# Kernel tuning notes

Hardware: AMD Instinct MI355X
Metric: run time of the kernel (lower is better)

The kernel has to match this reference:

```python
import jax, jax.numpy as jnp
import numpy as np

ENTRY_SIZE = 8192
TUPLE_SIZE = 16
N_NEURONS = ENTRY_SIZE // TUPLE_SIZE            # 512
ADDR_SPACE = 2 ** TUPLE_SIZE                     # 65536
BATCH = 4096


def setup_inputs() -> dict:
    key = jax.random.key(0)
    k1, k2, k3 = jax.random.split(key, 3)
    # Binary input bits [B, entry_size]
    inp = jax.random.randint(k1, (BATCH, ENTRY_SIZE), 0, 2, dtype=jnp.int32)
    # Permutation mapping bits -> tuples (identity permutation; arange fill)
    tuple_mapping = jnp.arange(ENTRY_SIZE, dtype=jnp.int64)
    # Dense RAM tables emulating the per-neuron dicts:
    #   counts[n, a] = number of training samples that hit address a in neuron n
    #                  (0 means the address was never trained -> not in dict)
    #   sums[n, a]   = accumulated target sum for that address
    counts = jax.random.randint(k2, (N_NEURONS, ADDR_SPACE), 0, 4, dtype=jnp.int32)
    sums = jax.random.normal(k3, (N_NEURONS, ADDR_SPACE), dtype=jnp.float32)
    return {"input": inp, "tuple_mapping": tuple_mapping, "counts": counts, "sums": sums}


def reference(input, tuple_mapping, counts, sums):
    """RegressionWisard.predict with centrality='mean'.

    input:  [B, entry_size] binary bits (int32)
    tuple_mapping: [entry_size] permutation (int)
    counts: [n_neurons, 2^tuple_size] int32 RAM hit counts
    sums:   [n_neurons, 2^tuple_size] float32 RAM target sums
    """
    B = input.shape[0]
    # Map and group bits into tuples: [B, N, T]
    mapped = jnp.take(input, tuple_mapping, axis=1).reshape(B, N_NEURONS, TUPLE_SIZE)
    # Binary address per (sample, neuron); tidx flips so bit 0 is the MSB.
    pow2 = (jnp.int32(1) << jnp.arange(TUPLE_SIZE - 1, -1, -1, dtype=jnp.int32))
    addr = jnp.einsum("bnt,t->bn", mapped, pow2)  # [B, N], values in [0, 2^T)
    neuron_idx = jnp.arange(N_NEURONS, dtype=jnp.int32)[None, :]  # [1, N]
    c = counts[neuron_idx, addr]  # [B, N]
    s = sums[neuron_idx, addr]    # [B, N]
    trained = c > 0               # dict-membership (torch.isin) equivalent
    response = jnp.sum(jnp.where(trained, s, jnp.float32(0)), axis=1)      # [B]
    counters = jnp.sum(jnp.where(trained, c, 0), axis=1).astype(s.dtype)   # [B]
    return jnp.nan_to_num(response / counters)
```

## Files before the change

### kernel.cpp

```cpp
#include <hip/hip_runtime.h>


constexpr int BATCH   = 4096;
constexpr int ENTRY   = 8192;
constexpr int TUP     = 16;
constexpr int NEUR    = ENTRY / TUP;
constexpr int LINES   = 4096;
constexpr int THREADS = 256;
constexpr int SPLIT   = 2;
constexpr int SB      = BATCH / SPLIT;
constexpr int EPT     = SB / THREADS;

typedef int v4i __attribute__((ext_vector_type(4)));

__device__ __forceinline__ int tuple_addr(
    const int* __restrict__ input, const int* __restrict__ map_n,
    int m0, bool contig, int s)
{
    if (contig) {
        const v4i* p = reinterpret_cast<const v4i*>(input + (size_t)s * ENTRY + m0);
        const v4i a0 = __builtin_nontemporal_load(p);
        const v4i a1 = __builtin_nontemporal_load(p + 1);
        const v4i a2 = __builtin_nontemporal_load(p + 2);
        const v4i a3 = __builtin_nontemporal_load(p + 3);
        return ((a0.x & 1) << 15) | ((a0.y & 1) << 14)
             | ((a0.z & 1) << 13) | ((a0.w & 1) << 12)
             | ((a1.x & 1) << 11) | ((a1.y & 1) << 10)
             | ((a1.z & 1) <<  9) | ((a1.w & 1) <<  8)
             | ((a2.x & 1) <<  7) | ((a2.y & 1) <<  6)
             | ((a2.z & 1) <<  5) | ((a2.w & 1) <<  4)
             | ((a3.x & 1) <<  3) | ((a3.y & 1) <<  2)
             | ((a3.z & 1) <<  1) |  (a3.w & 1);
    } else {
        const int* row = input + (size_t)s * ENTRY;
        int a = 0;
        #pragma unroll
        for (int t = 0; t < TUP; ++t) a = (a << 1) | (row[map_n[t]] & 1);
        return a;
    }
}

__global__ __launch_bounds__(THREADS) void wisard_addr(
    const int* __restrict__ input,
    const int* __restrict__ mapping,
    unsigned short* __restrict__ addr_t)
{
    const int tid  = threadIdx.x;
    const int lane = tid & 63;
    const int w    = tid >> 6;
    const int nch  = blockIdx.x & 7;
    const int sc   = blockIdx.x >> 3;
    const int s    = sc * 64 + lane;
    const int nb   = nch * 64 + w * 16;

    #pragma unroll 4
    for (int i = 0; i < 16; ++i) {
        const int n = __builtin_amdgcn_readfirstlane(nb) + i;
        const int* map_n = mapping + n * TUP;
        const int m0 = map_n[0];
        bool contig = ((m0 & 3) == 0);
        #pragma unroll
        for (int t = 1; t < TUP; ++t) contig &= (map_n[t] == m0 + t);
        const int a = tuple_addr(input, map_n, m0, contig, s);
        addr_t[(size_t)n * BATCH + s] = (unsigned short)a;
    }
}

__global__ __launch_bounds__(THREADS) void wisard_sortgather(
    const unsigned short* __restrict__ addr_t,
    const int*   __restrict__ counts,
    const float* __restrict__ sums,
    float2*      __restrict__ contrib)
{
    __shared__ unsigned int hist[LINES];
    __shared__ unsigned int sorted[SB];
    __shared__ unsigned int ttot[THREADS];
    __shared__ unsigned int wsum[THREADS / 64];

    const int tid   = threadIdx.x;
    const int lane  = tid & 63;
    const int w     = tid >> 6;
    const int n     = blockIdx.x >> 1;
    const int half  = blockIdx.x & 1;
    const int sbase = half * SB;

    unsigned int a[EPT];
    #pragma unroll
    for (int j = 0; j < EPT; ++j)
        a[j] = addr_t[(size_t)n * BATCH + sbase + j * THREADS + tid];

    #pragma unroll
    for (int j = 0; j < LINES / THREADS; ++j) hist[j * THREADS + tid] = 0u;
    __syncthreads();
    #pragma unroll
    for (int j = 0; j < EPT; ++j) atomicAdd(&hist[a[j] >> 4], 1u);
    __syncthreads();

    unsigned int loc[16];
    unsigned int run = 0;
    #pragma unroll
    for (int j = 0; j < 16; ++j) { loc[j] = run; run += hist[tid * 16 + j]; }
    ttot[tid] = run;
    __syncthreads();
    unsigned int v = ttot[tid];
    #pragma unroll
    for (int off = 1; off < 64; off <<= 1) {
        const unsigned int u = __shfl_up(v, off, 64);
        if (lane >= off) v += u;
    }
    if (lane == 63) wsum[w] = v;
    __syncthreads();
    unsigned int woff = 0;
    for (int i = 0; i < w; ++i) woff += wsum[i];
    const unsigned int excl = woff + v - ttot[tid];
    __syncthreads();
    #pragma unroll
    for (int j = 0; j < 16; ++j) hist[tid * 16 + j] = excl + loc[j];
    __syncthreads();

    #pragma unroll
    for (int j = 0; j < EPT; ++j) {
        const unsigned int pos = atomicAdd(&hist[a[j] >> 4], 1u);
        sorted[pos] = (a[j] << 12) | (unsigned int)(sbase + j * THREADS + tid);
    }
    __syncthreads();

    unsigned int pk[EPT];
    int   cv[EPT];
    float sv[EPT];
    #pragma unroll
    for (int j = 0; j < EPT; ++j) pk[j] = sorted[j * THREADS + tid];
    #pragma unroll
    for (int j = 0; j < EPT; ++j) {
        const size_t idx = ((size_t)n << 16) | (pk[j] >> 12);
        cv[j] = counts[idx];
        sv[j] = sums[idx];
    }
    #pragma unroll
    for (int j = 0; j < EPT; ++j) {
        const int sm = (int)(pk[j] & 4095u);
        const bool t = cv[j] > 0;
        float2 o;
        o.x = t ? sv[j] : 0.0f;
        o.y = __int_as_float(t ? cv[j] : 0);
        contrib[(size_t)n * BATCH + sm] = o;
    }
}

__global__ __launch_bounds__(THREADS) void wisard_final(
    const float2* __restrict__ contrib,
    float*        __restrict__ out)
{
    __shared__ float sr [4][64];
    __shared__ int   scn[4][64];
    const int tid  = threadIdx.x;
    const int lane = tid & 63;
    const int w    = tid >> 6;
    const int s    = blockIdx.x * 64 + lane;

    float r = 0.0f; int c = 0;
    #pragma unroll 8
    for (int i = 0; i < NEUR / 4; ++i) {
        const int n = w * (NEUR / 4) + i;
        const float2 vv = contrib[(size_t)n * BATCH + s];
        r += vv.x;
        c += __float_as_int(vv.y);
    }
    sr[w][lane] = r; scn[w][lane] = c;
    __syncthreads();
    if (w == 0) {
        r = sr[0][lane] + sr[1][lane] + sr[2][lane] + sr[3][lane];
        c = scn[0][lane] + scn[1][lane] + scn[2][lane] + scn[3][lane];
        out[s] = (c > 0) ? (r / (float)c) : 0.0f;
    }
}

__global__ __launch_bounds__(THREADS) void wisard_fallback(
    const int*   __restrict__ input,
    const int*   __restrict__ mapping,
    const int*   __restrict__ counts,
    const float* __restrict__ sums,
    float*       __restrict__ out)
{
    __shared__ float s_resp[2][THREADS / 64];
    __shared__ int   s_cnt [2][THREADS / 64];

    const int tid  = threadIdx.x;
    const int lane = tid & 63;
    const int wv   = tid >> 6;
    const int b0   = blockIdx.x * 2;

    int   cv[2][2];
    float sv[2][2];

    #pragma unroll
    for (int k = 0; k < 2; ++k) {
        const int n = tid + k * THREADS;
        const int* map_n = mapping + n * TUP;
        const int m0 = map_n[0];
        bool contig = ((m0 & 3) == 0);
        #pragma unroll
        for (int t = 1; t < TUP; ++t) contig &= (map_n[t] == m0 + t);
        #pragma unroll
        for (int s = 0; s < 2; ++s) {
            const int a = tuple_addr(input, map_n, m0, contig, b0 + s);
            const size_t idx = ((size_t)n << 16) | (unsigned)a;
            cv[s][k] = counts[idx];
            sv[s][k] = sums[idx];
        }
    }

    float resp[2]; int cnt[2];
    #pragma unroll
    for (int s = 0; s < 2; ++s) {
        resp[s] = 0.0f; cnt[s] = 0;
        #pragma unroll
        for (int k = 0; k < 2; ++k) {
            const bool t = cv[s][k] > 0;
            resp[s] += t ? sv[s][k] : 0.0f;
            cnt [s] += t ? cv[s][k] : 0;
        }
    }
    #pragma unroll
    for (int s = 0; s < 2; ++s) {
        float r = resp[s]; int c = cnt[s];
        #pragma unroll
        for (int off = 32; off > 0; off >>= 1) {
            r += __shfl_down(r, off, 64);
            c += __shfl_down(c, off, 64);
        }
        if (lane == 0) { s_resp[s][wv] = r; s_cnt[s][wv] = c; }
    }
    __syncthreads();
    if (tid < 2) {
        float r = 0.0f; int c = 0;
        #pragma unroll
        for (int w = 0; w < THREADS / 64; ++w) { r += s_resp[tid][w]; c += s_cnt[tid][w]; }
        out[b0 + tid] = (c > 0) ? (r / (float)c) : 0.0f;
    }
}

extern "C" void kernel_launch(void* const* d_in, const int* in_sizes, int n_in,
                              void* d_out, int out_size, void* d_ws, size_t ws_size,
                              hipStream_t stream) {
    (void)in_sizes; (void)n_in; (void)out_size;
    const int*   input   = (const int*)d_in[0];
    const int*   mapping = (const int*)d_in[1];
    const int*   counts  = (const int*)d_in[2];
    const float* sums    = (const float*)d_in[3];
    float*       out     = (float*)d_out;

    const size_t contrib_bytes = (size_t)NEUR * BATCH * sizeof(float2);
    const size_t addr_bytes    = (size_t)NEUR * BATCH * sizeof(unsigned short);

    if (ws_size < contrib_bytes + addr_bytes || d_ws == nullptr) {
        wisard_fallback<<<BATCH / 2, THREADS, 0, stream>>>(
            input, mapping, counts, sums, out);
        return;
    }

    float2*         contrib = (float2*)d_ws;
    unsigned short* addr_t  = (unsigned short*)((char*)d_ws + contrib_bytes);

    wisard_addr<<<(BATCH / 64) * 8, THREADS, 0, stream>>>(input, mapping, addr_t);
    wisard_sortgather<<<NEUR * SPLIT, THREADS, 0, stream>>>(
        addr_t, counts, sums, contrib);
    wisard_final<<<BATCH / 64, THREADS, 0, stream>>>(contrib, out);
}
```

Baseline: 414.5 us.

## Stream full RAM table lines per neuron instead of gathering sorted addresses

The gather kernel is replaced by one block per neuron over the full batch. Each thread reads one whole 64-byte line of counts and sums with nontemporal vector loads, then hands its values to the samples bucketed into that line through the shared-memory counting sort, accumulating into a shared contrib buffer. The address kernel now writes a sample-major layout so that input reads are coalesced across neurons. This swaps the scattered, partly coalesced table gathers for a fully contiguous sweep of both tables. The cost is extra bytes read for untouched lines, strided address reads in the stream kernel, and a serial per-line loop whose trip count varies between lanes.

New measurement: 390.2 us. 5.9% less time.

```diff
diff --git a/kernel.cpp b/kernel.cpp
--- a/kernel.cpp
+++ b/kernel.cpp
@@ -7,9 +7,6 @@
 constexpr int NEUR    = ENTRY / TUP;
 constexpr int LINES   = 4096;
 constexpr int THREADS = 256;
-constexpr int SPLIT   = 2;
-constexpr int SB      = BATCH / SPLIT;
-constexpr int EPT     = SB / THREADS;
 
 typedef int v4i __attribute__((ext_vector_type(4)));
 
@@ -40,62 +37,71 @@
     }
 }
 
+__device__ __forceinline__ int sel4(v4i v, int e01) {
+    const int ab = (e01 & 1) ? v.y : v.x;
+    const int cd = (e01 & 1) ? v.w : v.z;
+    return (e01 & 2) ? cd : ab;
+}
+__device__ __forceinline__ int sel16(v4i v0, v4i v1, v4i v2, v4i v3, int e) {
+    const int e2 = e & 3;
+    const int a = sel4(v0, e2), b = sel4(v1, e2);
+    const int c = sel4(v2, e2), d = sel4(v3, e2);
+    const int ab = (e & 4) ? b : a;
+    const int cd = (e & 4) ? d : c;
+    return (e & 8) ? cd : ab;
+}
+
 __global__ __launch_bounds__(THREADS) void wisard_addr(
     const int* __restrict__ input,
     const int* __restrict__ mapping,
     unsigned short* __restrict__ addr_t)
 {
-    const int tid  = threadIdx.x;
-    const int lane = tid & 63;
-    const int w    = tid >> 6;
-    const int nch  = blockIdx.x & 7;
-    const int sc   = blockIdx.x >> 3;
-    const int s    = sc * 64 + lane;
-    const int nb   = nch * 64 + w * 16;
-
-    #pragma unroll 4
-    for (int i = 0; i < 16; ++i) {
-        const int n = __builtin_amdgcn_readfirstlane(nb) + i;
+    const int lane = threadIdx.x & 63;
+    const int w    = threadIdx.x >> 6;
+    const int s    = blockIdx.x * 4 + w;
+
+    #pragma unroll 2
+    for (int j = 0; j < NEUR / 64; ++j) {
+        const int n = j * 64 + lane;
         const int* map_n = mapping + n * TUP;
         const int m0 = map_n[0];
         bool contig = ((m0 & 3) == 0);
         #pragma unroll
         for (int t = 1; t < TUP; ++t) contig &= (map_n[t] == m0 + t);
         const int a = tuple_addr(input, map_n, m0, contig, s);
-        addr_t[(size_t)n * BATCH + s] = (unsigned short)a;
-    }
-}
-
-__global__ __launch_bounds__(THREADS) void wisard_sortgather(
+        addr_t[(size_t)s * NEUR + n] = (unsigned short)a;
+    }
+}
+
+__global__ __launch_bounds__(THREADS) void wisard_stream(
     const unsigned short* __restrict__ addr_t,
     const int*   __restrict__ counts,
     const float* __restrict__ sums,
     float2*      __restrict__ contrib)
 {
     __shared__ unsigned int hist[LINES];
-    __shared__ unsigned int sorted[SB];
-    __shared__ unsigned int ttot[THREADS];
-    __shared__ unsigned int wsum[THREADS / 64];
-
-    const int tid   = threadIdx.x;
-    const int lane  = tid & 63;
-    const int w     = tid >> 6;
-    const int n     = blockIdx.x >> 1;
-    const int half  = blockIdx.x & 1;
-    const int sbase = half * SB;
-
-    unsigned int a[EPT];
-    #pragma unroll
-    for (int j = 0; j < EPT; ++j)
-        a[j] = addr_t[(size_t)n * BATCH + sbase + j * THREADS + tid];
+    __shared__ unsigned int sorted[BATCH];
+    __shared__ float2 acc[BATCH];
+
+    const int tid  = threadIdx.x;
+    const int lane = tid & 63;
+    const int w    = tid >> 6;
+    const int n = (blockIdx.x & 7) * 64 + (blockIdx.x >> 3);
+
+    unsigned int a[16];
+    #pragma unroll
+    for (int j = 0; j < 16; ++j)
+        a[j] = addr_t[(size_t)(j * THREADS + tid) * NEUR + n];
 
     #pragma unroll
     for (int j = 0; j < LINES / THREADS; ++j) hist[j * THREADS + tid] = 0u;
     __syncthreads();
     #pragma unroll
-    for (int j = 0; j < EPT; ++j) atomicAdd(&hist[a[j] >> 4], 1u);
-    __syncthreads();
-
+    for (int j = 0; j < 16; ++j) atomicAdd(&hist[a[j] >> 4], 1u);
+    __syncthreads();
+
+    unsigned int* ttot = reinterpret_cast<unsigned int*>(acc);
+    unsigned int* wsum = ttot + THREADS;
     unsigned int loc[16];
     unsigned int run = 0;
     #pragma unroll
@@ -112,38 +118,58 @@
     __syncthreads();
     unsigned int woff = 0;
     for (int i = 0; i < w; ++i) woff += wsum[i];
-    const unsigned int excl = woff + v - ttot[tid];
-    __syncthreads();
+    const unsigned int excl = woff + v - run;
     #pragma unroll
     for (int j = 0; j < 16; ++j) hist[tid * 16 + j] = excl + loc[j];
     __syncthreads();
 
     #pragma unroll
-    for (int j = 0; j < EPT; ++j) {
+    for (int j = 0; j < 16; ++j) {
         const unsigned int pos = atomicAdd(&hist[a[j] >> 4], 1u);
-        sorted[pos] = (a[j] << 12) | (unsigned int)(sbase + j * THREADS + tid);
-    }
-    __syncthreads();
-
-    unsigned int pk[EPT];
-    int   cv[EPT];
-    float sv[EPT];
-    #pragma unroll
-    for (int j = 0; j < EPT; ++j) pk[j] = sorted[j * THREADS + tid];
-    #pragma unroll
-    for (int j = 0; j < EPT; ++j) {
-        const size_t idx = ((size_t)n << 16) | (pk[j] >> 12);
-        cv[j] = counts[idx];
-        sv[j] = sums[idx];
-    }
-    #pragma unroll
-    for (int j = 0; j < EPT; ++j) {
-        const int sm = (int)(pk[j] & 4095u);
-        const bool t = cv[j] > 0;
-        float2 o;
-        o.x = t ? sv[j] : 0.0f;
-        o.y = __int_as_float(t ? cv[j] : 0);
-        contrib[(size_t)n * BATCH + sm] = o;
+        sorted[pos] = (a[j] << 12) | (unsigned int)(j * THREADS + tid);
+    }
+    __syncthreads();
+
+    #pragma unroll
+    for (int j = 0; j < 16; ++j) acc[j * THREADS + tid] = make_float2(0.0f, 0.0f);
+    __syncthreads();
+
+    const size_t tbase = (size_t)n << 16;
+    for (int j = 0; j < 16; ++j) {
+        const int L = j * THREADS + tid;
+        const v4i* cp = reinterpret_cast<const v4i*>(counts + tbase + ((size_t)L << 4));
+        const v4i* sp = reinterpret_cast<const v4i*>(
+            reinterpret_cast<const int*>(sums) + tbase + ((size_t)L << 4));
+        const v4i c0 = __builtin_nontemporal_load(cp);
+        const v4i c1 = __builtin_nontemporal_load(cp + 1);
+        const v4i c2 = __builtin_nontemporal_load(cp + 2);
+        const v4i c3 = __builtin_nontemporal_load(cp + 3);
+        const v4i s0 = __builtin_nontemporal_load(sp);
+        const v4i s1 = __builtin_nontemporal_load(sp + 1);
+        const v4i s2 = __builtin_nontemporal_load(sp + 2);
+        const v4i s3 = __builtin_nontemporal_load(sp + 3);
+        const unsigned int beg = (L == 0) ? 0u : hist[L - 1];
+        const unsigned int end = hist[L];
+        for (unsigned int k = beg; k < end; ++k) {
+            const unsigned int pk = sorted[k];
+            const int e  = (int)((pk >> 12) & 15u);
+            const int sm = (int)(pk & 4095u);
+            const int cv = sel16(c0, c1, c2, c3, e);
+            const int sb = sel16(s0, s1, s2, s3, e);
+            if (cv > 0) {
+                float2 o;
+                o.x = __int_as_float(sb);
+                o.y = __int_as_float(cv);
+                acc[sm] = o;
+            }
+        }
+    }
+    __syncthreads();
+
+    #pragma unroll
+    for (int j = 0; j < 16; ++j) {
+        const int s = j * THREADS + tid;
+        contrib[(size_t)n * BATCH + s] = acc[s];
     }
 }
 
@@ -251,7 +277,7 @@
     float*       out     = (float*)d_out;
 
     const size_t contrib_bytes = (size_t)NEUR * BATCH * sizeof(float2);
-    const size_t addr_bytes    = (size_t)NEUR * BATCH * sizeof(unsigned short);
+    const size_t addr_bytes    = (size_t)BATCH * NEUR * sizeof(unsigned short);
 
     if (ws_size < contrib_bytes + addr_bytes || d_ws == nullptr) {
         wisard_fallback<<<BATCH / 2, THREADS, 0, stream>>>(
@@ -262,8 +288,7 @@
     float2*         contrib = (float2*)d_ws;
     unsigned short* addr_t  = (unsigned short*)((char*)d_ws + contrib_bytes);
 
-    wisard_addr<<<(BATCH / 64) * 8, THREADS, 0, stream>>>(input, mapping, addr_t);
-    wisard_sortgather<<<NEUR * SPLIT, THREADS, 0, stream>>>(
-        addr_t, counts, sums, contrib);
+    wisard_addr<<<BATCH / 4, THREADS, 0, stream>>>(input, mapping, addr_t);
+    wisard_stream<<<NEUR, THREADS, 0, stream>>>(addr_t, counts, sums, contrib);
     wisard_final<<<BATCH / 64, THREADS, 0, stream>>>(contrib, out);
 }
```
